# Optimization experiments

Measured on AMD Instinct MI355X. Metric: run time of the kernel, lower is better.

Reference implementation:

```python
import jax, jax.numpy as jnp
import numpy as np

D_MODEL = 2048
N_HEADS = 16
D_K = D_MODEL // N_HEADS
MAX_SEQ_LEN = 2048


def _rotary_tables(dim, max_seq_len):
    angular_freq = (1.0 / 10000.0) ** jnp.linspace(0.0, 1.0, dim // 2, dtype=jnp.float32)
    t = jnp.arange(max_seq_len, dtype=jnp.float32)
    theta = jnp.einsum('i,j->ij', t, angular_freq)  # [S, dk/2]
    return jnp.cos(theta), jnp.sin(theta)


def _apply_rotary(x, cos, sin):
    # x: [B, H, S, dk]; cos/sin: [S, dk/2]
    seq_len = x.shape[-2]
    c = cos[:seq_len][None, None]
    s = sin[:seq_len][None, None]
    x1, x2 = jnp.split(x, 2, axis=-1)
    y1 = x1 * c - x2 * s
    y2 = x1 * s + x2 * c
    return jnp.concatenate([y1, y2], axis=-1).astype(x.dtype)


def setup_inputs() -> dict:
    key = jax.random.key(0)
    k_x, k_qkv, k_o = jax.random.split(key, 3)
    B, S = 2, 2048
    x = jax.random.normal(k_x, (B, S, D_MODEL), dtype=jnp.float32)
    scale = 1.0 / np.sqrt(D_MODEL)
    w_qkv = jax.random.normal(k_qkv, (3 * D_MODEL, D_MODEL), dtype=jnp.float32) * scale
    w_o = jax.random.normal(k_o, (D_MODEL, D_MODEL), dtype=jnp.float32) * scale
    return {"x": x, "w_qkv": w_qkv, "w_o": w_o}


def reference(x, w_qkv, w_o):
    B, S, _ = x.shape
    cos, sin = _rotary_tables(D_K, MAX_SEQ_LEN)
    qkv = jnp.einsum('bsd,ed->bse', x, w_qkv)  # [B, S, 3*d_model]
    qkv = qkv.reshape(B, S, 3, N_HEADS, D_K).transpose(2, 0, 3, 1, 4)  # [3,B,H,S,dk]
    Q, K, V = qkv[0], qkv[1], qkv[2]
    Q = _apply_rotary(Q, cos, sin)
    K = _apply_rotary(K, cos, sin)
    scale = 1.0 / np.sqrt(D_K)
    scores = jnp.einsum('bhqd,bhkd->bhqk', Q, K) * scale
    causal = jnp.tril(jnp.ones((S, S), dtype=bool))
    scores = jnp.where(causal[None, None], scores, jnp.finfo(scores.dtype).min)
    attn = jax.nn.softmax(scores, axis=-1)
    out = jnp.einsum('bhqk,bhkd->bhqd', attn, V)  # [B,H,S,dk]
    out = out.transpose(0, 2, 1, 3).reshape(B, S, D_MODEL)
    return jnp.einsum('bsd,ed->bse', out, w_o)
```

## Files before the change

kernel.cpp:

```cpp
#include <hip/hip_runtime.h>
#include <hip/hip_bf16.h>


typedef __bf16 bf16;
typedef __bf16 bf16x4 __attribute__((ext_vector_type(4)));
typedef __bf16 bf16x8 __attribute__((ext_vector_type(8)));
typedef float f32x4 __attribute__((ext_vector_type(4)));
typedef float f32x16 __attribute__((ext_vector_type(16)));
typedef int i32x4 __attribute__((ext_vector_type(4)));

#define DEV __device__ __forceinline__

DEV void gll16(const void* g, void* lds_base_wave_uniform) {
  __builtin_amdgcn_global_load_lds((const __attribute__((address_space(1))) void*)g,
                                   (__attribute__((address_space(3))) void*)lds_base_wave_uniform,
                                   16, 0, 0);
}

DEV f32x4 mfma16(bf16x8 a, bf16x8 b, f32x4 c) {
  return __builtin_amdgcn_mfma_f32_16x16x32_bf16(a, b, c, 0, 0, 0);
}
DEV f32x16 mfma32(bf16x8 a, bf16x8 b, f32x16 c) {
  return __builtin_amdgcn_mfma_f32_32x32x16_bf16(a, b, c, 0, 0, 0);
}

DEV int cvtpk(float lo, float hi) {
  int r;
  asm("v_cvt_pk_bf16_f32 %0, %1, %2" : "=v"(r) : "v"(lo), "v"(hi));
  return r;
}

__global__ __launch_bounds__(256) void prep_all(const float* __restrict__ x,
                                                const float* __restrict__ wqkv,
                                                const float* __restrict__ wo,
                                                bf16* __restrict__ xb,
                                                bf16* __restrict__ wqkvb,
                                                bf16* __restrict__ wob,
                                                float* __restrict__ ctab,
                                                float* __restrict__ stab) {
  const int b = blockIdx.x;
  if (b < 12288) {
    const float* in;
    bf16* out;
    int bb = b;
    if (b < 4096) {
      in = x; out = xb;
    } else if (b < 10240) {
      in = wqkv; out = wqkvb; bb -= 4096;
    } else {
      in = wo; out = wob; bb -= 10240;
    }
    const int i = (bb * 256 + threadIdx.x) << 3;
    float4 a = *(const float4*)(in + i);
    float4 c = *(const float4*)(in + i + 4);
    bf16x8 o;
    o[0] = (bf16)a.x; o[1] = (bf16)a.y; o[2] = (bf16)a.z; o[3] = (bf16)a.w;
    o[4] = (bf16)c.x; o[5] = (bf16)c.y; o[6] = (bf16)c.z; o[7] = (bf16)c.w;
    *(bf16x8*)(out + i) = o;
  } else {
    const int id = (b - 12288) * 256 + threadIdx.x;
    const int s = id >> 6, j = id & 63;
    float freq = powf(10000.0f, -(float)j / 63.0f);
    float th = (float)s * freq;
    ctab[id] = cosf(th);
    stab[id] = sinf(th);
  }
}

__global__ __launch_bounds__(512, 2) void gemm384(const bf16* __restrict__ A,
                                                  const bf16* __restrict__ Bt,
                                                  bf16* __restrict__ q_out,
                                                  bf16* __restrict__ k_out,
                                                  bf16* __restrict__ v_out,
                                                  const float* __restrict__ ctab,
                                                  const float* __restrict__ stab) {
  constexpr int K = 2048, NKT = 64;
  constexpr int BUFB = 40960;
  __shared__ char lds[3 * BUFB];
  const int id = blockIdx.x;
  const int swz = (id & 7) * 32 + (id >> 3);
  const int bx = swz & 15, by = swz >> 4;
  const int m0 = by << 8;
  const int n0 = bx * 384;
  const int tid = threadIdx.x, w = tid >> 6, l = tid & 63;
  const int wm = w >> 2, wn = w & 3;
  const int lsl = (l & 7) ^ ((l >> 3) & 7);
  const int srow = ((l >> 3) << 1) + (lsl >> 2);
  const int scol = (lsl & 3) << 3;

  auto STAGE = [&](int t, char* base) {
    const int k0 = t << 5;
#pragma unroll
    for (int c = 0; c < 2; ++c) {
      const int row = (c << 7) + (w << 4) + srow;
      gll16(A + (size_t)(m0 + row) * K + k0 + scol, base + (c << 13) + (w << 10));
    }
#pragma unroll
    for (int c = 0; c < 3; ++c) {
      const int row = (c << 7) + (w << 4) + srow;
      gll16(Bt + (size_t)(n0 + row) * K + k0 + scol, base + 16384 + (c << 13) + (w << 10));
    }
  };

  f32x4 acc[8][6] = {};

  STAGE(0, (char*)lds);
  STAGE(1, (char*)lds + BUFB);
  asm volatile("s_waitcnt vmcnt(5)" ::: "memory");
  __builtin_amdgcn_s_barrier();

#pragma unroll 1
  for (int t = 0, bi = 0, bj = 2; t < NKT; ++t) {
    char* rbase = (char*)lds + bi * BUFB;
    bf16x8 bfr[6];
#pragma unroll
    for (int j = 0; j < 6; ++j) {
      const int row = ((j >> 1) << 7) + ((j & 1) << 6) + (wn << 4) + (l & 15);
      const int sr = row >> 1;
      bfr[j] = *(const bf16x8*)(rbase + 16384 + sr * 128 +
                                (((((row & 1) << 2) | (l >> 4)) ^ (sr & 7)) << 4));
    }
    bf16x8 af[4];
#pragma unroll
    for (int i = 0; i < 4; ++i) {
      const int row = (wm << 7) + (i << 4) + (l & 15);
      const int sr = row >> 1;
      af[i] = *(const bf16x8*)(rbase + sr * 128 +
                               (((((row & 1) << 2) | (l >> 4)) ^ (sr & 7)) << 4));
    }
    if (t + 2 < NKT) STAGE(t + 2, (char*)lds + bj * BUFB);
    asm volatile("s_waitcnt lgkmcnt(0)" ::: "memory");
    __builtin_amdgcn_sched_barrier(0);
    __builtin_amdgcn_s_setprio(1);
#pragma unroll
    for (int i = 0; i < 4; ++i)
#pragma unroll
      for (int j = 0; j < 6; ++j)
        acc[i][j] = mfma16(af[i], bfr[j], acc[i][j]);
    __builtin_amdgcn_s_setprio(0);
#pragma unroll
    for (int i = 0; i < 4; ++i) {
      const int row = (wm << 7) + 64 + (i << 4) + (l & 15);
      const int sr = row >> 1;
      af[i] = *(const bf16x8*)(rbase + sr * 128 +
                               (((((row & 1) << 2) | (l >> 4)) ^ (sr & 7)) << 4));
    }
    asm volatile("s_waitcnt lgkmcnt(0)" ::: "memory");
    __builtin_amdgcn_sched_barrier(0);
    __builtin_amdgcn_s_setprio(1);
#pragma unroll
    for (int i = 0; i < 4; ++i)
#pragma unroll
      for (int j = 0; j < 6; ++j)
        acc[4 + i][j] = mfma16(af[i], bfr[j], acc[4 + i][j]);
    __builtin_amdgcn_s_setprio(0);
    if (t + 2 < NKT) {
      asm volatile("s_waitcnt vmcnt(5)" ::: "memory");
    } else if (t + 2 == NKT) {
      asm volatile("s_waitcnt vmcnt(0)" ::: "memory");
    }
    __builtin_amdgcn_sched_barrier(0);
    __builtin_amdgcn_s_barrier();
    bi = (bi == 2) ? 0 : bi + 1;
    bj = (bj == 2) ? 0 : bj + 1;
  }

  const int d2 = (wn << 4) + (l & 15);
#pragma unroll
  for (int i = 0; i < 8; ++i) {
    const int mbase = m0 + (wm << 7) + (i << 4) + ((l >> 4) << 2);
    const int b_ = mbase >> 11, sbase = mbase & 2047;
    float cc[4], ss[4];
    if (((n0 + 256) >> 11) == 1 || (n0 >> 11) == 1) {
#pragma unroll
      for (int r = 0; r < 4; ++r) {
        cc[r] = ctab[((sbase + r) << 6) + d2];
        ss[r] = stab[((sbase + r) << 6) + d2];
      }
    }
#pragma unroll
    for (int p = 0; p < 3; ++p) {
      const int nb = n0 + (p << 7);
      const int which = nb >> 11;
      const int h = (nb >> 7) & 15;
      if (which == 0) {
        const size_t base = (((size_t)((b_ << 4) | h)) * 2048 + sbase) * 128;
#pragma unroll
        for (int r = 0; r < 4; ++r) {
          q_out[base + ((size_t)r << 7) + d2]      = (bf16)acc[i][2 * p][r];
          q_out[base + ((size_t)r << 7) + d2 + 64] = (bf16)acc[i][2 * p + 1][r];
        }
      } else if (which == 1) {
        const size_t base = (((size_t)((b_ << 4) | h)) * 2048 + sbase) * 128;
#pragma unroll
        for (int r = 0; r < 4; ++r) {
          const float x1 = acc[i][2 * p][r], x2 = acc[i][2 * p + 1][r];
          k_out[base + ((size_t)r << 7) + d2]      = (bf16)(x1 * cc[r] - x2 * ss[r]);
          k_out[base + ((size_t)r << 7) + d2 + 64] = (bf16)(x1 * ss[r] + x2 * cc[r]);
        }
      } else {
        bf16x4 v1, v2;
#pragma unroll
        for (int r = 0; r < 4; ++r) {
          v1[r] = (bf16)acc[i][2 * p][r];
          v2[r] = (bf16)acc[i][2 * p + 1][r];
        }
        const size_t hb = ((size_t)((b_ << 4) | h) << 18);
        *(bf16x4*)(v_out + hb + ((size_t)d2 << 11) + sbase) = v1;
        *(bf16x4*)(v_out + hb + ((size_t)(d2 + 64) << 11) + sbase) = v2;
      }
    }
  }
}

template <int NTN>
__global__ __launch_bounds__(256, 2) void gemm_o(const bf16* __restrict__ A,
                                                 const bf16* __restrict__ Bt,
                                                 float* __restrict__ f_out) {
  constexpr int K = 2048, NKT = 64;
  constexpr int BUFB = 16384;
  __shared__ char lds[3 * BUFB];
  const int nwg = 32 * NTN;
  const int id = blockIdx.x;
  const int swz = (id & 7) * (nwg >> 3) + (id >> 3);
  const int bx = swz % NTN, by = swz / NTN;
  const int m0 = by << 7, n0 = bx << 7;
  const int tid = threadIdx.x, w = tid >> 6, l = tid & 63;
  const int wm = w >> 1, wn = w & 1;
  const int lsl = (l & 7) ^ ((l >> 3) & 7);
  const int srow = ((l >> 3) << 1) + (lsl >> 2);
  const int scol = (lsl & 3) << 3;

  auto STAGE = [&](int t, char* base) {
    const int k0 = t << 5;
#pragma unroll
    for (int c = 0; c < 2; ++c) {
      const int row = (c << 6) + (w << 4) + srow;
      gll16(A + (size_t)(m0 + row) * K + k0 + scol, base + (c << 12) + (w << 10));
      gll16(Bt + (size_t)(n0 + row) * K + k0 + scol, base + 8192 + (c << 12) + (w << 10));
    }
  };

  f32x4 acc[4][4] = {};

  STAGE(0, (char*)lds);
  STAGE(1, (char*)lds + BUFB);
  asm volatile("s_waitcnt vmcnt(4)" ::: "memory");
  __builtin_amdgcn_s_barrier();

#pragma unroll 1
  for (int t = 0, bi = 0, bj = 2; t < NKT; ++t) {
    char* rbase = (char*)lds + bi * BUFB;
    bf16x8 af[4], bfr[4];
#pragma unroll
    for (int i = 0; i < 4; ++i) {
      const int row = (wm << 6) + (i << 4) + (l & 15);
      const int sr = row >> 1;
      af[i] = *(const bf16x8*)(rbase + sr * 128 +
                               (((((row & 1) << 2) | (l >> 4)) ^ (sr & 7)) << 4));
    }
#pragma unroll
    for (int j = 0; j < 4; ++j) {
      const int row = (wn << 6) + (j << 4) + (l & 15);
      const int sr = row >> 1;
      bfr[j] = *(const bf16x8*)(rbase + 8192 + sr * 128 +
                                (((((row & 1) << 2) | (l >> 4)) ^ (sr & 7)) << 4));
    }
    if (t + 2 < NKT) STAGE(t + 2, (char*)lds + bj * BUFB);
    asm volatile("s_waitcnt lgkmcnt(0)" ::: "memory");
    __builtin_amdgcn_sched_barrier(0);
    __builtin_amdgcn_s_setprio(1);
#pragma unroll
    for (int i = 0; i < 4; ++i)
#pragma unroll
      for (int j = 0; j < 4; ++j)
        acc[i][j] = mfma16(af[i], bfr[j], acc[i][j]);
    __builtin_amdgcn_s_setprio(0);
    if (t + 2 < NKT) {
      asm volatile("s_waitcnt vmcnt(4)" ::: "memory");
    } else if (t + 2 == NKT) {
      asm volatile("s_waitcnt vmcnt(0)" ::: "memory");
    }
    __builtin_amdgcn_sched_barrier(0);
    __builtin_amdgcn_s_barrier();
    bi = (bi == 2) ? 0 : bi + 1;
    bj = (bj == 2) ? 0 : bj + 1;
  }

#pragma unroll
  for (int i = 0; i < 4; ++i)
#pragma unroll
    for (int j = 0; j < 4; ++j)
#pragma unroll
      for (int r = 0; r < 4; ++r) {
        const int m = m0 + (wm << 6) + (i << 4) + ((l >> 4) << 2) + r;
        const int n = n0 + (wn << 6) + (j << 4) + (l & 15);
        f_out[(size_t)m * 2048 + n] = acc[i][j][r];
      }
}

__global__ __launch_bounds__(256, 2) void attn_kernel(const bf16* __restrict__ Qb,
                                                      const bf16* __restrict__ Kb,
                                                      const bf16* __restrict__ Vt,
                                                      bf16* __restrict__ Ao,
                                                      const float* __restrict__ ctab,
                                                      const float* __restrict__ stab) {
  constexpr int S = 2048;
  __shared__ bf16 Ks[3][64 * 128];
  __shared__ bf16 Vs[3][128 * 64];
  const int id = blockIdx.x;
  const int swz = (id & 7) * 32 + (id >> 3);
  const int bh = swz >> 3;
  const int pp = swz & 7;
  const int ntA = (pp + 1) << 1;
  const int NT = 34;
  const int tid = threadIdx.x, w = tid >> 6, l = tid & 63;
  const int hi = l >> 5;
  const bf16* Qp = Qb + ((size_t)bh << 18);
  const bf16* Kp = Kb + ((size_t)bh << 18);
  const bf16* Vp = Vt + ((size_t)bh << 18);

  auto KVSEQ = [&](int ti) { return ((ti < ntA) ? ti : ti - ntA) << 6; };

  auto STAGE_KV = [&](int kv0, int bufi) {
    char* Kbase = (char*)Ks + bufi * 16384;
    char* Vbase = (char*)Vs + bufi * 16384;
#pragma unroll
    for (int i = 0; i < 4; ++i) {
      const int rk = (w << 4) + (i << 2) + (l >> 4);
      gll16(Kp + ((size_t)(kv0 + rk) << 7) + (((l & 15) ^ (rk & 7)) << 3),
            Kbase + (w << 12) + (i << 10));
      const int rv = (w << 5) + (i << 3) + (l >> 3);
      gll16(Vp + (size_t)rv * S + kv0 + (((l & 7) ^ (rv & 7)) << 3),
            Vbase + (w << 12) + (i << 10));
    }
  };

  bf16x8 qf[8];
  auto LOAD_Q = [&](int q0_) {
    const int sq = q0_ + (w << 5) + (l & 31);
#pragma unroll
    for (int kt = 0; kt < 8; ++kt)
      qf[kt] = *(const bf16x8*)(Qp + ((size_t)sq << 7) + (kt << 4) + (hi << 3));
    const float QS = 0.08838834764831845f * 1.4426950408889634f;
#pragma unroll
    for (int kt = 0; kt < 4; ++kt) {
      const int d2 = (kt << 4) + (hi << 3);
      const float* cp = ctab + (sq << 6) + d2;
      const float* sp = stab + (sq << 6) + d2;
      float4 c0 = *(const float4*)cp, c1 = *(const float4*)(cp + 4);
      float4 s0 = *(const float4*)sp, s1 = *(const float4*)(sp + 4);
      const float cA[8] = {c0.x, c0.y, c0.z, c0.w, c1.x, c1.y, c1.z, c1.w};
      const float sA[8] = {s0.x, s0.y, s0.z, s0.w, s1.x, s1.y, s1.z, s1.w};
      const bf16x8 lo = qf[kt], up = qf[kt + 4];
#pragma unroll
      for (int j2 = 0; j2 < 8; ++j2) {
        const float a = (float)lo[j2], b2 = (float)up[j2];
        qf[kt][j2]     = (bf16)((a * cA[j2] - b2 * sA[j2]) * QS);
        qf[kt + 4][j2] = (bf16)((a * sA[j2] + b2 * cA[j2]) * QS);
      }
    }
  };

  f32x16 o[4] = {};
  float mrun = -3e38f, lrun = 0.f;
  int q0 = pp << 7;

  auto EPILOGUE = [&](int q0_) {
    const float rinv = 1.0f / lrun;
    const int b = bh >> 4, h = bh & 15;
    const int sq = q0_ + (w << 5) + (l & 31);
    bf16* Arow = Ao + (((size_t)(b * S + sq)) << 11) + (h << 7);
#pragma unroll
    for (int dt = 0; dt < 4; ++dt)
#pragma unroll
      for (int g = 0; g < 4; ++g) {
        bf16x4 ov;
#pragma unroll
        for (int r = 0; r < 4; ++r) ov[r] = (bf16)(o[dt][(g << 2) + r] * rinv);
        *(bf16x4*)(Arow + (dt << 5) + (g << 3) + (hi << 2)) = ov;
      }
  };

  LOAD_Q(q0);
  STAGE_KV(KVSEQ(0), 0);
  STAGE_KV(KVSEQ(1), 1);
  asm volatile("s_waitcnt vmcnt(8)" ::: "memory");
  __builtin_amdgcn_sched_barrier(0);
  __builtin_amdgcn_s_barrier();

  int rb = 0;
#pragma unroll 1
  for (int ti = 0; ti < NT; ++ti) {
    if (ti + 2 < NT) {
      const int sb = (rb == 0) ? 2 : rb - 1;
      STAGE_KV(KVSEQ(ti + 2), sb);
    }
    const int kv0 = KVSEQ(ti);
    const int qminw = q0 + (w << 5);
    if (kv0 <= qminw + 31) {
      const char* Kbase = (const char*)Ks + rb * 16384;
      const char* Vbase = (const char*)Vs + rb * 16384;
      f32x16 sc0 = {}, sc1 = {};
      __builtin_amdgcn_s_setprio(1);
#pragma unroll
      for (int kt = 0; kt < 8; ++kt) {
        const int rk0 = l & 31;
        const int coff = ((kt << 5) + (hi << 4));
        bf16x8 k0 = *(const bf16x8*)(Kbase + (rk0 << 8) + (coff ^ ((rk0 & 7) << 4)));
        bf16x8 k1 = *(const bf16x8*)(Kbase + ((rk0 + 32) << 8) + (coff ^ ((rk0 & 7) << 4)));
        sc0 = mfma32(k0, qf[kt], sc0);
        sc1 = mfma32(k1, qf[kt], sc1);
      }
      __builtin_amdgcn_s_setprio(0);
      if (kv0 + 63 > qminw) {
        const int qg = qminw + (l & 31);
#pragma unroll
        for (int r = 0; r < 16; ++r) {
          const int kvr = kv0 + (r & 3) + ((r >> 2) << 3) + (hi << 2);
          if (kvr > qg) sc0[r] = -3e38f;
          if (kvr + 32 > qg) sc1[r] = -3e38f;
        }
      }
      f32x16 mm;
#pragma unroll
      for (int r = 0; r < 16; ++r) mm[r] = fmaxf(sc0[r], sc1[r]);
#pragma unroll
      for (int off = 8; off; off >>= 1)
#pragma unroll
        for (int r = 0; r < off; ++r) mm[r] = fmaxf(mm[r], mm[r + off]);
      float mx = mm[0];
      mx = fmaxf(mx, __shfl_xor(mx, 32));
      const float mnew = fmaxf(mrun, mx);
      if (!__all(mx <= mrun)) {
        const float alpha = exp2f(mrun - mnew);
        lrun *= alpha;
#pragma unroll
        for (int dt = 0; dt < 4; ++dt) o[dt] *= alpha;
      }
      mrun = mnew;
      float p0 = 0.f, p1 = 0.f, p2 = 0.f, p3 = 0.f;
#pragma unroll
      for (int r = 0; r < 16; r += 2) {
        sc0[r] = exp2f(sc0[r] - mnew); sc0[r + 1] = exp2f(sc0[r + 1] - mnew);
        sc1[r] = exp2f(sc1[r] - mnew); sc1[r + 1] = exp2f(sc1[r + 1] - mnew);
        p0 += sc0[r]; p1 += sc0[r + 1]; p2 += sc1[r]; p3 += sc1[r + 1];
      }
      float ps = (p0 + p1) + (p2 + p3);
      ps += __shfl_xor(ps, 32);
      lrun += ps;
#pragma unroll
      for (int ks = 0; ks < 4; ++ks) {
        const f32x16& s = (ks & 2) ? sc1 : sc0;
        const int rbp = (ks & 1) << 3;
        int pa_ = cvtpk(s[rbp + 0], s[rbp + 1]);
        int pb_ = cvtpk(s[rbp + 2], s[rbp + 3]);
        int pc_ = cvtpk(s[rbp + 4], s[rbp + 5]);
        int pd_ = cvtpk(s[rbp + 6], s[rbp + 7]);
        int sa = __shfl_xor(pa_, 32), sb2 = __shfl_xor(pb_, 32);
        int sc_ = __shfl_xor(pc_, 32), sd = __shfl_xor(pd_, 32);
        i32x4 pi;
        pi[0] = hi ? sc_ : pa_;
        pi[1] = hi ? sd : pb_;
        pi[2] = hi ? pc_ : sa;
        pi[3] = hi ? pd_ : sb2;
        const bf16x8 pf = __builtin_bit_cast(bf16x8, pi);
        __builtin_amdgcn_s_setprio(1);
#pragma unroll
        for (int dt = 0; dt < 4; ++dt) {
          const int rd = (dt << 5) + (l & 31);
          const bf16x8 vf = *(const bf16x8*)(Vbase + (rd << 7) +
                                             (((ks << 5) + (hi << 4)) ^ ((rd & 7) << 4)));
          o[dt] = mfma32(vf, pf, o[dt]);
        }
        __builtin_amdgcn_s_setprio(0);
      }
    }
    if (ti == ntA - 1) {
      EPILOGUE(q0);
      q0 = (15 - pp) << 7;
#pragma unroll
      for (int dt = 0; dt < 4; ++dt)
#pragma unroll
        for (int r = 0; r < 16; ++r) o[dt][r] = 0.f;
      mrun = -3e38f; lrun = 0.f;
      LOAD_Q(q0);
    }
    if (ti + 2 < NT) {
      asm volatile("s_waitcnt vmcnt(8)" ::: "memory");
    } else if (ti + 2 == NT) {
      asm volatile("s_waitcnt vmcnt(0)" ::: "memory");
    }
    __builtin_amdgcn_sched_barrier(0);
    __builtin_amdgcn_s_barrier();
    rb = (rb == 2) ? 0 : rb + 1;
  }
  EPILOGUE(q0);
}

extern "C" void kernel_launch(void* const* d_in, const int* in_sizes, int n_in,
                              void* d_out, int out_size, void* d_ws, size_t ws_size,
                              hipStream_t stream) {
  const float* x = (const float*)d_in[0];
  const float* w_qkv = (const float*)d_in[1];
  const float* w_o = (const float*)d_in[2];
  float* out = (float*)d_out;
  char* ws = (char*)d_ws;

  bf16* xb    = (bf16*)(ws);
  bf16* wqkvb = (bf16*)(ws + (16ull << 20));
  bf16* wob   = (bf16*)(ws + (40ull << 20));
  bf16* Qb    = (bf16*)(ws + (48ull << 20));
  bf16* Kb    = (bf16*)(ws + (64ull << 20));
  bf16* Vt    = (bf16*)(ws + (80ull << 20));
  bf16* Ao    = (bf16*)(ws + (96ull << 20));
  float* ctab = (float*)(ws + (112ull << 20));
  float* stab = (float*)(ws + (113ull << 20));

  prep_all<<<12800, 256, 0, stream>>>(x, w_qkv, w_o, xb, wqkvb, wob, ctab, stab);
  gemm384<<<256, 512, 0, stream>>>(xb, wqkvb, Qb, Kb, Vt, ctab, stab);
  attn_kernel<<<256, 256, 0, stream>>>(Qb, Kb, Vt, Ao, ctab, stab);
  gemm_o<16><<<512, 256, 0, stream>>>(Ao, wob, out);
}
```

Baseline: 259.6 us.

## Split attention KV range across two blocks and merge with combine kernel

Replaces the paired-q-tile attention kernel, which ran 256 blocks with a triple-buffered KV pipeline, with a split-KV version. It launches 1024 blocks, each covering half of one q-tile's causal KV range with a single LDS buffer, and raises the launch-bounds occupancy hint from 2 to 4. A new combine kernel merges the two partial outputs using the saved per-row max and sum. The aim is more parallelism and occupancy, at the cost of losing the async prefetch overlap, an extra launch, and the traffic to write and reread bf16 partials. Storing the unnormalized partials in bf16 may also lose precision.

```diff
diff --git a/kernel.cpp b/kernel.cpp
--- a/kernel.cpp
+++ b/kernel.cpp
@@ -299,49 +299,50 @@
       }
 }
 
-__global__ __launch_bounds__(256, 2) void attn_kernel(const bf16* __restrict__ Qb,
-                                                      const bf16* __restrict__ Kb,
-                                                      const bf16* __restrict__ Vt,
-                                                      bf16* __restrict__ Ao,
-                                                      const float* __restrict__ ctab,
-                                                      const float* __restrict__ stab) {
+__global__ __launch_bounds__(256, 4) void attn_split(const bf16* __restrict__ Qb,
+                                                     const bf16* __restrict__ Kb,
+                                                     const bf16* __restrict__ Vt,
+                                                     bf16* __restrict__ po,
+                                                     float* __restrict__ pm,
+                                                     float* __restrict__ pl,
+                                                     const float* __restrict__ ctab,
+                                                     const float* __restrict__ stab) {
   constexpr int S = 2048;
-  __shared__ bf16 Ks[3][64 * 128];
-  __shared__ bf16 Vs[3][128 * 64];
+  __shared__ bf16 Ks[64 * 128];
+  __shared__ bf16 Vs[128 * 64];
   const int id = blockIdx.x;
-  const int swz = (id & 7) * 32 + (id >> 3);
-  const int bh = swz >> 3;
-  const int pp = swz & 7;
-  const int ntA = (pp + 1) << 1;
-  const int NT = 34;
+  const int c = id & 7, inner = id >> 3;
+  const int g = inner >> 5, a = inner & 31;
+  const int bh = (c << 2) | g;
+  const int qt = ((a & 15) + (g << 2)) & 15;
+  const int half = (a >> 4) ^ (g & 1);
+  const int T = qt + 1;
+  const int kvbase = half * T;
+  const int q0 = qt << 7;
   const int tid = threadIdx.x, w = tid >> 6, l = tid & 63;
   const int hi = l >> 5;
   const bf16* Qp = Qb + ((size_t)bh << 18);
   const bf16* Kp = Kb + ((size_t)bh << 18);
   const bf16* Vp = Vt + ((size_t)bh << 18);
 
-  auto KVSEQ = [&](int ti) { return ((ti < ntA) ? ti : ti - ntA) << 6; };
-
-  auto STAGE_KV = [&](int kv0, int bufi) {
-    char* Kbase = (char*)Ks + bufi * 16384;
-    char* Vbase = (char*)Vs + bufi * 16384;
+  auto STAGE_KV = [&](int kv0) {
 #pragma unroll
     for (int i = 0; i < 4; ++i) {
       const int rk = (w << 4) + (i << 2) + (l >> 4);
       gll16(Kp + ((size_t)(kv0 + rk) << 7) + (((l & 15) ^ (rk & 7)) << 3),
-            Kbase + (w << 12) + (i << 10));
+            (char*)Ks + (w << 12) + (i << 10));
       const int rv = (w << 5) + (i << 3) + (l >> 3);
       gll16(Vp + (size_t)rv * S + kv0 + (((l & 7) ^ (rv & 7)) << 3),
-            Vbase + (w << 12) + (i << 10));
+            (char*)Vs + (w << 12) + (i << 10));
     }
   };
 
+  const int sq = q0 + (w << 5) + (l & 31);
   bf16x8 qf[8];
-  auto LOAD_Q = [&](int q0_) {
-    const int sq = q0_ + (w << 5) + (l & 31);
-#pragma unroll
-    for (int kt = 0; kt < 8; ++kt)
-      qf[kt] = *(const bf16x8*)(Qp + ((size_t)sq << 7) + (kt << 4) + (hi << 3));
+#pragma unroll
+  for (int kt = 0; kt < 8; ++kt)
+    qf[kt] = *(const bf16x8*)(Qp + ((size_t)sq << 7) + (kt << 4) + (hi << 3));
+  {
     const float QS = 0.08838834764831845f * 1.4426950408889634f;
 #pragma unroll
     for (int kt = 0; kt < 4; ++kt) {
@@ -355,60 +356,31 @@
       const bf16x8 lo = qf[kt], up = qf[kt + 4];
 #pragma unroll
       for (int j2 = 0; j2 < 8; ++j2) {
-        const float a = (float)lo[j2], b2 = (float)up[j2];
-        qf[kt][j2]     = (bf16)((a * cA[j2] - b2 * sA[j2]) * QS);
-        qf[kt + 4][j2] = (bf16)((a * sA[j2] + b2 * cA[j2]) * QS);
-      }
-    }
-  };
+        const float aa = (float)lo[j2], b2 = (float)up[j2];
+        qf[kt][j2]     = (bf16)((aa * cA[j2] - b2 * sA[j2]) * QS);
+        qf[kt + 4][j2] = (bf16)((aa * sA[j2] + b2 * cA[j2]) * QS);
+      }
+    }
+  }
 
   f32x16 o[4] = {};
   float mrun = -3e38f, lrun = 0.f;
-  int q0 = pp << 7;
-
-  auto EPILOGUE = [&](int q0_) {
-    const float rinv = 1.0f / lrun;
-    const int b = bh >> 4, h = bh & 15;
-    const int sq = q0_ + (w << 5) + (l & 31);
-    bf16* Arow = Ao + (((size_t)(b * S + sq)) << 11) + (h << 7);
-#pragma unroll
-    for (int dt = 0; dt < 4; ++dt)
-#pragma unroll
-      for (int g = 0; g < 4; ++g) {
-        bf16x4 ov;
-#pragma unroll
-        for (int r = 0; r < 4; ++r) ov[r] = (bf16)(o[dt][(g << 2) + r] * rinv);
-        *(bf16x4*)(Arow + (dt << 5) + (g << 3) + (hi << 2)) = ov;
-      }
-  };
-
-  LOAD_Q(q0);
-  STAGE_KV(KVSEQ(0), 0);
-  STAGE_KV(KVSEQ(1), 1);
-  asm volatile("s_waitcnt vmcnt(8)" ::: "memory");
-  __builtin_amdgcn_sched_barrier(0);
-  __builtin_amdgcn_s_barrier();
-
-  int rb = 0;
+  const int qminw = q0 + (w << 5);
+
 #pragma unroll 1
-  for (int ti = 0; ti < NT; ++ti) {
-    if (ti + 2 < NT) {
-      const int sb = (rb == 0) ? 2 : rb - 1;
-      STAGE_KV(KVSEQ(ti + 2), sb);
-    }
-    const int kv0 = KVSEQ(ti);
-    const int qminw = q0 + (w << 5);
+  for (int t = 0; t < T; ++t) {
+    const int kv0 = (kvbase + t) << 6;
+    STAGE_KV(kv0);
+    __syncthreads();
     if (kv0 <= qminw + 31) {
-      const char* Kbase = (const char*)Ks + rb * 16384;
-      const char* Vbase = (const char*)Vs + rb * 16384;
       f32x16 sc0 = {}, sc1 = {};
       __builtin_amdgcn_s_setprio(1);
 #pragma unroll
       for (int kt = 0; kt < 8; ++kt) {
         const int rk0 = l & 31;
         const int coff = ((kt << 5) + (hi << 4));
-        bf16x8 k0 = *(const bf16x8*)(Kbase + (rk0 << 8) + (coff ^ ((rk0 & 7) << 4)));
-        bf16x8 k1 = *(const bf16x8*)(Kbase + ((rk0 + 32) << 8) + (coff ^ ((rk0 & 7) << 4)));
+        bf16x8 k0 = *(const bf16x8*)((const char*)Ks + (rk0 << 8) + (coff ^ ((rk0 & 7) << 4)));
+        bf16x8 k1 = *(const bf16x8*)((const char*)Ks + ((rk0 + 32) << 8) + (coff ^ ((rk0 & 7) << 4)));
         sc0 = mfma32(k0, qf[kt], sc0);
         sc1 = mfma32(k1, qf[kt], sc1);
       }
@@ -469,33 +441,53 @@
 #pragma unroll
         for (int dt = 0; dt < 4; ++dt) {
           const int rd = (dt << 5) + (l & 31);
-          const bf16x8 vf = *(const bf16x8*)(Vbase + (rd << 7) +
+          const bf16x8 vf = *(const bf16x8*)((const char*)Vs + (rd << 7) +
                                              (((ks << 5) + (hi << 4)) ^ ((rd & 7) << 4)));
           o[dt] = mfma32(vf, pf, o[dt]);
         }
         __builtin_amdgcn_s_setprio(0);
       }
     }
-    if (ti == ntA - 1) {
-      EPILOGUE(q0);
-      q0 = (15 - pp) << 7;
-#pragma unroll
-      for (int dt = 0; dt < 4; ++dt)
-#pragma unroll
-        for (int r = 0; r < 16; ++r) o[dt][r] = 0.f;
-      mrun = -3e38f; lrun = 0.f;
-      LOAD_Q(q0);
-    }
-    if (ti + 2 < NT) {
-      asm volatile("s_waitcnt vmcnt(8)" ::: "memory");
-    } else if (ti + 2 == NT) {
-      asm volatile("s_waitcnt vmcnt(0)" ::: "memory");
-    }
-    __builtin_amdgcn_sched_barrier(0);
-    __builtin_amdgcn_s_barrier();
-    rb = (rb == 2) ? 0 : rb + 1;
-  }
-  EPILOGUE(q0);
+    __syncthreads();
+  }
+
+  const int qrow = (bh << 11) + sq;
+  bf16* Prow = po + ((size_t)half << 23) + ((size_t)qrow << 7);
+#pragma unroll
+  for (int dt = 0; dt < 4; ++dt)
+#pragma unroll
+    for (int gg = 0; gg < 4; ++gg) {
+      bf16x4 ov;
+#pragma unroll
+      for (int r = 0; r < 4; ++r) ov[r] = (bf16)o[dt][(gg << 2) + r];
+      *(bf16x4*)(Prow + (dt << 5) + (gg << 3) + (hi << 2)) = ov;
+    }
+  if (hi == 0) {
+    pm[(half << 16) + qrow] = mrun;
+    pl[(half << 16) + qrow] = lrun;
+  }
+}
+
+__global__ __launch_bounds__(256) void attn_combine(const bf16* __restrict__ po,
+                                                    const float* __restrict__ pm,
+                                                    const float* __restrict__ pl,
+                                                    bf16* __restrict__ Ao) {
+  const int id = blockIdx.x * 256 + threadIdx.x;
+  const int qrow = id >> 4, dc = id & 15;
+  const float m0 = pm[qrow], m1 = pm[65536 + qrow];
+  const float l0 = pl[qrow], l1 = pl[65536 + qrow];
+  const float ms = fmaxf(m0, m1);
+  float a0 = exp2f(m0 - ms), a1 = exp2f(m1 - ms);
+  const float rinv = 1.0f / (l0 * a0 + l1 * a1);
+  a0 *= rinv; a1 *= rinv;
+  const bf16x8 o0 = *(const bf16x8*)(po + ((size_t)qrow << 7) + (dc << 3));
+  const bf16x8 o1 = *(const bf16x8*)(po + (1ull << 23) + ((size_t)qrow << 7) + (dc << 3));
+  bf16x8 out;
+#pragma unroll
+  for (int j = 0; j < 8; ++j) out[j] = (bf16)((float)o0[j] * a0 + (float)o1[j] * a1);
+  const int bh = qrow >> 11, sl = qrow & 2047;
+  const int b = bh >> 4, h = bh & 15;
+  *(bf16x8*)(Ao + (((size_t)(b * 2048 + sl)) << 11) + (h << 7) + (dc << 3)) = out;
 }
 
 extern "C" void kernel_launch(void* const* d_in, const int* in_sizes, int n_in,
@@ -516,9 +508,13 @@
   bf16* Ao    = (bf16*)(ws + (96ull << 20));
   float* ctab = (float*)(ws + (112ull << 20));
   float* stab = (float*)(ws + (113ull << 20));
+  bf16* po  = (bf16*)(ws);
+  float* pm = (float*)(ws + (32ull << 20));
+  float* pl = (float*)(ws + (33ull << 20));
 
   prep_all<<<12800, 256, 0, stream>>>(x, w_qkv, w_o, xb, wqkvb, wob, ctab, stab);
   gemm384<<<256, 512, 0, stream>>>(xb, wqkvb, Qb, Kb, Vt, ctab, stab);
-  attn_kernel<<<256, 256, 0, stream>>>(Qb, Kb, Vt, Ao, ctab, stab);
+  attn_split<<<1024, 256, 0, stream>>>(Qb, Kb, Vt, po, pm, pl, ctab, stab);
+  attn_combine<<<4096, 256, 0, stream>>>(po, pm, pl, Ao);
   gemm_o<16><<<512, 256, 0, stream>>>(Ao, wob, out);
 }
```

Result: slower. 381.6 us (+47.0%).
